# Kernel optimization log

Measured on AMD Instinct MI355X. Metric: run time of the kernel, lower is better.

The kernel has to match this reference:

```python
import jax, jax.numpy as jnp
import numpy as np

EMBED_DIM = 32  # module-level constant used for the 1/sqrt(d) scale in the source
DROP_P = 0.2


def setup_inputs() -> dict:
    key = jax.random.key(0)
    kx, kq, kk, kv = jax.random.split(key, 4)
    B, T, C = 8, 4096, EMBED_DIM
    x = jax.random.normal(kx, (B, T, C), dtype=jnp.float32)
    Wq = jax.random.normal(kq, (C, C), dtype=jnp.float32) * (1.0 / np.sqrt(C))
    Wk = jax.random.normal(kk, (C, C), dtype=jnp.float32) * (1.0 / np.sqrt(C))
    Wv = jax.random.normal(kv, (C, C), dtype=jnp.float32) * (1.0 / np.sqrt(C))
    return {"x": x, "Wq": Wq, "Wk": Wk, "Wv": Wv}


def reference(x, Wq, Wk, Wv):
    B, T, C = x.shape
    # bias-free linear projections: y = x @ W.T (torch nn.Linear convention)
    q = jnp.einsum('btc,dc->btd', x, Wq)
    k = jnp.einsum('btc,dc->btd', x, Wk)
    v = jnp.einsum('btc,dc->btd', x, Wv)
    # scaled scores [B, T, T]
    att = jnp.einsum('btd,bsd->bts', q, k) / jnp.sqrt(jnp.float32(EMBED_DIM))
    causal = jnp.tril(jnp.ones((T, T), dtype=bool))
    att = jnp.where(causal, att, -jnp.inf)
    wei = jax.nn.softmax(att, axis=-1)
    # dropout on attention weights (training mode, p=0.2), deterministic key
    keep = jax.random.bernoulli(jax.random.key(42), 1.0 - DROP_P, wei.shape)
    wei = jnp.where(keep, wei / (1.0 - DROP_P), 0.0)
    return jnp.einsum('bts,bsd->btd', wei, v)
```

## Files before the change

### kernel.cpp

```cpp
#include <hip/hip_runtime.h>
#include <stdint.h>

#define BB 8
#define TTN 4096
#define CCH 32
#define WIN 128
#define KEEP_LT9 3435974144u

typedef __attribute__((ext_vector_type(8))) short bf16x8;
typedef __attribute__((ext_vector_type(4))) float f32x4;

union B8 { uint32_t u[4]; uint4 q; bf16x8 v; };

__device__ __forceinline__ uint32_t cvt_pk_bf16(float lo, float hi) {
    uint32_t d;
    asm("v_cvt_pk_bf16_f32 %0, %1, %2" : "=v"(d) : "v"(lo), "v"(hi));
    return d;
}

__device__ __forceinline__ uint32_t rotl32(uint32_t x, int r) {
    return __builtin_amdgcn_alignbit(x, x, 32 - r);
}

__device__ __forceinline__ void threefry4(uint32_t i0, uint32_t i1, uint32_t i2, uint32_t i3,
                                          uint32_t& o0, uint32_t& o1, uint32_t& o2, uint32_t& o3) {
    const uint32_t K2 = 42u ^ 0x1BD11BDAu;
    uint32_t a0 = 0u, a1 = 0u, a2 = 0u, a3 = 0u;
    uint32_t b0 = i0 + 42u, b1 = i1 + 42u, b2 = i2 + 42u, b3 = i3 + 42u;
#define R4(r)                                                                  \
    { a0 += b0; a1 += b1; a2 += b2; a3 += b3;                                  \
      b0 = rotl32(b0, (r)); b1 = rotl32(b1, (r));                              \
      b2 = rotl32(b2, (r)); b3 = rotl32(b3, (r));                              \
      b0 ^= a0; b1 ^= a1; b2 ^= a2; b3 ^= a3; }
#define INJ(da, db)                                                            \
    { a0 += (da); a1 += (da); a2 += (da); a3 += (da);                          \
      b0 += (db); b1 += (db); b2 += (db); b3 += (db); }
    R4(13) R4(15) R4(26) R4(6)
    INJ(42u, K2 + 1u)
    R4(17) R4(29) R4(16) R4(24)
    INJ(K2, 2u)
    R4(13) R4(15) R4(26) R4(6)
    INJ(0u, 42u + 3u)
    R4(17) R4(29) R4(16) R4(24)
    INJ(42u, K2 + 4u)
    R4(13) R4(15) R4(26) R4(6)
    INJ(K2, 5u)
#undef R4
#undef INJ
    o0 = a0 ^ b0; o1 = a1 ^ b1; o2 = a2 ^ b2; o3 = a3 ^ b3;
}

__global__ __launch_bounds__(256) void proj_qkv(const float* __restrict__ x,
                                                const float* __restrict__ Wq,
                                                const float* __restrict__ Wk,
                                                const float* __restrict__ Wv,
                                                float* __restrict__ Qf,
                                                uint16_t* __restrict__ Kb,
                                                uint16_t* __restrict__ Vt) {
    __shared__ float sW[3][CCH * CCH];
    __shared__ uint16_t vs[256][34];
    const int tid = threadIdx.x;
    for (int i = tid; i < CCH * CCH; i += 256) {
        sW[0][i] = Wq[i]; sW[1][i] = Wk[i]; sW[2][i] = Wv[i];
    }
    __syncthreads();
    const int row = blockIdx.x * 256 + tid;
    const float4* xp = reinterpret_cast<const float4*>(x + (size_t)row * CCH);
    float xr[CCH];
    #pragma unroll
    for (int i = 0; i < 8; ++i) {
        float4 t4 = xp[i];
        xr[4*i] = t4.x; xr[4*i+1] = t4.y; xr[4*i+2] = t4.z; xr[4*i+3] = t4.w;
    }
    const float scale = 0.17677669529663687f;
    #pragma unroll
    for (int mtx = 0; mtx < 3; ++mtx) {
        float o[CCH];
        #pragma unroll
        for (int d = 0; d < CCH; ++d) {
            float s0 = 0.f, s1 = 0.f, s2 = 0.f, s3 = 0.f;
            #pragma unroll
            for (int c = 0; c < CCH; c += 4) {
                s0 += xr[c]   * sW[mtx][d*CCH + c];
                s1 += xr[c+1] * sW[mtx][d*CCH + c+1];
                s2 += xr[c+2] * sW[mtx][d*CCH + c+2];
                s3 += xr[c+3] * sW[mtx][d*CCH + c+3];
            }
            o[d] = (s0 + s1) + (s2 + s3);
            if (mtx == 0) o[d] *= scale;
        }
        if (mtx == 0) {
            float4* op = reinterpret_cast<float4*>(Qf + (size_t)row * CCH);
            #pragma unroll
            for (int i = 0; i < 8; ++i)
                op[i] = make_float4(o[4*i], o[4*i+1], o[4*i+2], o[4*i+3]);
        } else if (mtx == 1) {
            uint32_t dw[16];
            #pragma unroll
            for (int k = 0; k < 16; ++k) dw[k] = cvt_pk_bf16(o[2*k], o[2*k+1]);
            uint4* kp = reinterpret_cast<uint4*>((char*)Kb + (size_t)row * 64);
            #pragma unroll
            for (int q = 0; q < 4; ++q)
                kp[q] = make_uint4(dw[4*q], dw[4*q+1], dw[4*q+2], dw[4*q+3]);
        } else {
            #pragma unroll
            for (int k = 0; k < 16; ++k)
                *reinterpret_cast<uint32_t*>(&vs[tid][2*k]) = cvt_pk_bf16(o[2*k], o[2*k+1]);
        }
    }
    __syncthreads();
    const int b = blockIdx.x >> 4, seg = blockIdx.x & 15;
    const int d = tid >> 3, part = tid & 7;
    uint32_t dw[16];
    #pragma unroll
    for (int k = 0; k < 16; ++k) {
        const uint32_t lo = vs[part*32 + 2*k][d];
        const uint32_t hi = vs[part*32 + 2*k + 1][d];
        dw[k] = lo | (hi << 16);
    }
    uint16_t* dst = Vt + (size_t)b * (CCH * TTN) + (size_t)d * TTN + seg * 256 + part * 32;
    uint4* dp = reinterpret_cast<uint4*>(dst);
    #pragma unroll
    for (int q = 0; q < 4; ++q)
        dp[q] = make_uint4(dw[4*q], dw[4*q+1], dw[4*q+2], dw[4*q+3]);
}

__global__ __launch_bounds__(256, 8) void attn_mfma(const float* __restrict__ Qf,
                                                    const uint16_t* __restrict__ Kb,
                                                    const uint16_t* __restrict__ Vt,
                                                    float* __restrict__ out) {
    __shared__ __align__(16) char smem[4864];

    const int j = blockIdx.x;
    const int b = j & 7;
    const int thalf = (j >> 3) & 1;
    const int tile = 127 - (j >> 4);

    const int w = threadIdx.x >> 6;
    const int lane = threadIdx.x & 63;
    const int tl = lane & 15;
    const int g = lane >> 4;
    const int sg = w;
    const int slb = sg * 32;
    const int tbase = tile * 32 + thalf * 16;
    const int t_g = tbase + tl;

    const float* qrow = Qf + ((size_t)b * TTN + t_g) * CCH + g * 8;
    const float4 qa = *reinterpret_cast<const float4*>(qrow);
    const float4 qb = *reinterpret_cast<const float4*>(qrow + 4);
    B8 qf;
    qf.u[0] = cvt_pk_bf16(qa.x, qa.y); qf.u[1] = cvt_pk_bf16(qa.z, qa.w);
    qf.u[2] = cvt_pk_bf16(qb.x, qb.y); qf.u[3] = cvt_pk_bf16(qb.z, qb.w);

    f32x4 acc0 = {0.f,0.f,0.f,0.f}, acc1 = {0.f,0.f,0.f,0.f};
    float m = -1e30f, l = 0.f;

    const char* Kbb = (const char*)Kb + (size_t)b * TTN * 64;
    const char* Vbb = (const char*)Vt + (size_t)b * CCH * TTN * 2;
    const uint32_t idxb = ((uint32_t)b << 24) | ((uint32_t)t_g << 12);

    const int nwin = ((tbase + 15) >> 7) + 1;

#define ATT_WINDOW(S0, TAIL)                                                   \
    {                                                                          \
        const int srow = (S0) + slb;                                           \
        B8 ka, kc, va, vc, pf;                                                 \
        ka.q = *reinterpret_cast<const uint4*>(Kbb + (size_t)(srow + tl) * 64 + g * 16); \
        kc.q = *reinterpret_cast<const uint4*>(Kbb + (size_t)(srow + 16 + tl) * 64 + g * 16); \
        va.q = *reinterpret_cast<const uint4*>(Vbb + (size_t)tl * 8192 + (size_t)(srow + g * 8) * 2); \
        vc.q = *reinterpret_cast<const uint4*>(Vbb + (size_t)(16 + tl) * 8192 + (size_t)(srow + g * 8) * 2); \
               \
        const uint32_t ib = idxb | (uint32_t)(srow + 4 * g);                   \
        uint32_t r0, r1, r2, r3, r4, r5, r6, r7;                               \
        threefry4(ib,       ib + 1u,  ib + 2u,  ib + 3u,  r0, r1, r2, r3);     \
        threefry4(ib + 16u, ib + 17u, ib + 18u, ib + 19u, r4, r5, r6, r7);     \
        const f32x4 zz = {0.f,0.f,0.f,0.f};                                    \
        f32x4 d0 = __builtin_amdgcn_mfma_f32_16x16x32_bf16(ka.v, qf.v, zz, 0, 0, 0); \
        f32x4 d1 = __builtin_amdgcn_mfma_f32_16x16x32_bf16(kc.v, qf.v, zz, 0, 0, 0); \
        if (TAIL) {                                                            \
            const int sv = srow + 4 * g;                                       \
            d0.x = (sv + 0  <= t_g) ? d0.x : -1e30f;                           \
            d0.y = (sv + 1  <= t_g) ? d0.y : -1e30f;                           \
            d0.z = (sv + 2  <= t_g) ? d0.z : -1e30f;                           \
            d0.w = (sv + 3  <= t_g) ? d0.w : -1e30f;                           \
            d1.x = (sv + 16 <= t_g) ? d1.x : -1e30f;                           \
            d1.y = (sv + 17 <= t_g) ? d1.y : -1e30f;                           \
            d1.z = (sv + 18 <= t_g) ? d1.z : -1e30f;                           \
            d1.w = (sv + 19 <= t_g) ? d1.w : -1e30f;                           \
        }                                                                      \
        float mx = fmaxf(fmaxf(fmaxf(d0.x, d0.y), fmaxf(d0.z, d0.w)),          \
                         fmaxf(fmaxf(d1.x, d1.y), fmaxf(d1.z, d1.w)));         \
        mx = fmaxf(mx, __shfl_xor(mx, 16));                                    \
        mx = fmaxf(mx, __shfl_xor(mx, 32));                                    \
        const bool up = mx > m + 8.0f;               \
        const float corr = up ? __expf(m - mx) : 1.0f;                         \
        m = up ? mx : m;                                                       \
        l *= corr; acc0 *= corr; acc1 *= corr;                                 \
        float p0 = __expf(d0.x - m), p1 = __expf(d0.y - m);                    \
        float p2 = __expf(d0.z - m), p3 = __expf(d0.w - m);                    \
        float p4 = __expf(d1.x - m), p5 = __expf(d1.y - m);                    \
        float p6 = __expf(d1.z - m), p7 = __expf(d1.w - m);                    \
        if (TAIL) {                                                            \
            const float alive = (srow <= t_g) ? 1.0f : 0.0f;                   \
            p0 *= alive; p1 *= alive; p2 *= alive; p3 *= alive;                \
            p4 *= alive; p5 *= alive; p6 *= alive; p7 *= alive;                \
        }                                                                      \
        float ls = ((p0 + p1) + (p2 + p3)) + ((p4 + p5) + (p6 + p7));          \
        ls += __shfl_xor(ls, 16);                                              \
        ls += __shfl_xor(ls, 32);                                              \
        l += ls;                                                               \
        const float q0 = (r0 < KEEP_LT9) ? p0 : 0.f;        \
        const float q1 = (r1 < KEEP_LT9) ? p1 : 0.f;                           \
        const float q2 = (r2 < KEEP_LT9) ? p2 : 0.f;                           \
        const float q3 = (r3 < KEEP_LT9) ? p3 : 0.f;                           \
        const float q4 = (r4 < KEEP_LT9) ? p4 : 0.f;                           \
        const float q5 = (r5 < KEEP_LT9) ? p5 : 0.f;                           \
        const float q6 = (r6 < KEEP_LT9) ? p6 : 0.f;                           \
        const float q7 = (r7 < KEEP_LT9) ? p7 : 0.f;                           \
        const uint32_t k00 = cvt_pk_bf16(q0, q1), k01 = cvt_pk_bf16(q2, q3);   \
        const uint32_t k10 = cvt_pk_bf16(q4, q5), k11 = cvt_pk_bf16(q6, q7);   \
        const int srcA = 16 * ((g & 1) * 2) + tl;                              \
        const int srcB = srcA + 16;                                            \
        const uint32_t a0 = (uint32_t)__shfl((int)k00, srcA);                  \
        const uint32_t b0 = (uint32_t)__shfl((int)k10, srcA);                  \
        const uint32_t a1 = (uint32_t)__shfl((int)k01, srcA);                  \
        const uint32_t b1 = (uint32_t)__shfl((int)k11, srcA);                  \
        const uint32_t a2 = (uint32_t)__shfl((int)k00, srcB);                  \
        const uint32_t b2 = (uint32_t)__shfl((int)k10, srcB);                  \
        const uint32_t a3 = (uint32_t)__shfl((int)k01, srcB);                  \
        const uint32_t b3 = (uint32_t)__shfl((int)k11, srcB);                  \
        const bool hi = (g >= 2);                                              \
        pf.u[0] = hi ? b0 : a0; pf.u[1] = hi ? b1 : a1;                        \
        pf.u[2] = hi ? b2 : a2; pf.u[3] = hi ? b3 : a3;                        \
        acc0 = __builtin_amdgcn_mfma_f32_16x16x32_bf16(va.v, pf.v, acc0, 0, 0, 0); \
        acc1 = __builtin_amdgcn_mfma_f32_16x16x32_bf16(vc.v, pf.v, acc1, 0, 0, 0); \
    }

    #pragma unroll 1
    for (int win = 0; win < nwin - 1; ++win) {
        ATT_WINDOW(win << 7, 0)
    }
    {
        const int s0 = (nwin - 1) << 7;
        if (s0 + slb <= tbase + 15) ATT_WINDOW(s0, 1)
    }
#undef ATT_WINDOW

#define SLOT(S) reinterpret_cast<float*>(smem + (S) * 2432)
#define PUBLISH(SB)                                                            \
    {                                                                          \
        float* sb = (SB);                                                      \
        *reinterpret_cast<float4*>(sb + tl * 36 + 4 * g)      = make_float4(acc0.x, acc0.y, acc0.z, acc0.w); \
        *reinterpret_cast<float4*>(sb + tl * 36 + 16 + 4 * g) = make_float4(acc1.x, acc1.y, acc1.z, acc1.w); \
        if (g == 0) { sb[576 + 2 * tl] = m; sb[577 + 2 * tl] = l; }            \
    }
#define CONSUME(SB)                                                            \
    {                                                                          \
        const float* sb = (SB);                                                \
        const float m2 = sb[576 + 2 * tl], l2 = sb[577 + 2 * tl];              \
        const float4 x0 = *reinterpret_cast<const float4*>(sb + tl * 36 + 4 * g); \
        const float4 x1 = *reinterpret_cast<const float4*>(sb + tl * 36 + 16 + 4 * g); \
        const float mn = fmaxf(m, m2);                                         \
        const float ca = __expf(m - mn), cb = __expf(m2 - mn);                 \
        l = l * ca + l2 * cb;                                                  \
        acc0.x = acc0.x * ca + x0.x * cb; acc0.y = acc0.y * ca + x0.y * cb;    \
        acc0.z = acc0.z * ca + x0.z * cb; acc0.w = acc0.w * ca + x0.w * cb;    \
        acc1.x = acc1.x * ca + x1.x * cb; acc1.y = acc1.y * ca + x1.y * cb;    \
        acc1.z = acc1.z * ca + x1.z * cb; acc1.w = acc1.w * ca + x1.w * cb;    \
        m = mn;                                                                \
    }
    if (sg >= 2) PUBLISH(SLOT(sg - 2))
    __syncthreads();
    if (sg < 2) CONSUME(SLOT(sg))
    __syncthreads();
    if (sg == 1) PUBLISH(SLOT(0))
    __syncthreads();
    if (sg == 0) {
        CONSUME(SLOT(0))
        const float inv = 1.0f / (0.8f * l);
        float* orow = out + ((size_t)b * TTN + t_g) * CCH;
        *reinterpret_cast<float4*>(orow + 4 * g) =
            make_float4(acc0.x * inv, acc0.y * inv, acc0.z * inv, acc0.w * inv);
        *reinterpret_cast<float4*>(orow + 16 + 4 * g) =
            make_float4(acc1.x * inv, acc1.y * inv, acc1.z * inv, acc1.w * inv);
    }
#undef SLOT
#undef PUBLISH
#undef CONSUME
}

extern "C" void kernel_launch(void* const* d_in, const int* in_sizes, int n_in,
                              void* d_out, int out_size, void* d_ws, size_t ws_size,
                              hipStream_t stream) {
    const float* x  = (const float*)d_in[0];
    const float* Wq = (const float*)d_in[1];
    const float* Wk = (const float*)d_in[2];
    const float* Wv = (const float*)d_in[3];
    float* outp = (float*)d_out;

    float*    Qf = (float*)d_ws;
    uint16_t* Kb = (uint16_t*)((char*)d_ws + 4194304);
    uint16_t* Vt = (uint16_t*)((char*)d_ws + 6291456);

    proj_qkv<<<(BB * TTN) / 256, 256, 0, stream>>>(x, Wq, Wk, Wv, Qf, Kb, Vt);
    attn_mfma<<<2048, 256, 0, stream>>>(Qf, Kb, Vt, outp);
}
```

Baseline: 171.1 us.

## Prefetch next K/V window and RNG, use exp2 with folded log2e scale, LDS exchange

The attention loop now software-pipelines the work: the next window's K/V tiles are loaded and its threefry dropout bits computed before the current window's softmax and PV MFMAs run. The softmax switches to raw v_exp_f32 (base 2) by folding log2(e) into the Q scale. The per-lane row sum is deferred and reduced once after the loop. The cross-lane max and P-fragment exchanges use LDS instead of shuffles. This raises register pressure (occupancy hint drops from 8 to 6) and LDS use in exchange for hiding memory latency and cutting exp and shuffle cost.

Measured after the change: 164.7 us. 1.04x faster.

```diff
diff --git a/kernel.cpp b/kernel.cpp
--- a/kernel.cpp
+++ b/kernel.cpp
@@ -4,7 +4,6 @@
 #define BB 8
 #define TTN 4096
 #define CCH 32
-#define WIN 128
 #define KEEP_LT9 3435974144u
 
 typedef __attribute__((ext_vector_type(8))) short bf16x8;
@@ -15,6 +14,12 @@
 __device__ __forceinline__ uint32_t cvt_pk_bf16(float lo, float hi) {
     uint32_t d;
     asm("v_cvt_pk_bf16_f32 %0, %1, %2" : "=v"(d) : "v"(lo), "v"(hi));
+    return d;
+}
+
+__device__ __forceinline__ float exp2_fast(float x) {
+    float d;
+    asm("v_exp_f32 %0, %1" : "=v"(d) : "v"(x));
     return d;
 }
 
@@ -72,7 +77,7 @@
         float4 t4 = xp[i];
         xr[4*i] = t4.x; xr[4*i+1] = t4.y; xr[4*i+2] = t4.z; xr[4*i+3] = t4.w;
     }
-    const float scale = 0.17677669529663687f;
+    const float scale = 0.2550348616f;
     #pragma unroll
     for (int mtx = 0; mtx < 3; ++mtx) {
         float o[CCH];
@@ -125,11 +130,11 @@
         dp[q] = make_uint4(dw[4*q], dw[4*q+1], dw[4*q+2], dw[4*q+3]);
 }
 
-__global__ __launch_bounds__(256, 8) void attn_mfma(const float* __restrict__ Qf,
+__global__ __launch_bounds__(256, 6) void attn_mfma(const float* __restrict__ Qf,
                                                     const uint16_t* __restrict__ Kb,
                                                     const uint16_t* __restrict__ Vt,
                                                     float* __restrict__ out) {
-    __shared__ __align__(16) char smem[4864];
+    __shared__ __align__(16) char smem[9984];
 
     const int j = blockIdx.x;
     const int b = j & 7;
@@ -140,8 +145,7 @@
     const int lane = threadIdx.x & 63;
     const int tl = lane & 15;
     const int g = lane >> 4;
-    const int sg = w;
-    const int slb = sg * 32;
+    const int slb = w * 32;
     const int tbase = tile * 32 + thalf * 16;
     const int t_g = tbase + tl;
 
@@ -161,24 +165,33 @@
 
     const int nwin = ((tbase + 15) >> 7) + 1;
 
-#define ATT_WINDOW(S0, TAIL)                                                   \
+    float* mxex = reinterpret_cast<float*>(smem) + (w << 6);
+    uint32_t* pex = reinterpret_cast<uint32_t*>(smem + 1024) + (w << 8);
+
+    B8 kaA, kcA, vaA, vcA, kaB, kcB, vaB, vcB;
+    uint32_t rA[8], rB[8];
+
+#define LOADF(KA, KC, VA, VC, S0)                                              \
     {                                                                          \
         const int srow = (S0) + slb;                                           \
-        B8 ka, kc, va, vc, pf;                                                 \
-        ka.q = *reinterpret_cast<const uint4*>(Kbb + (size_t)(srow + tl) * 64 + g * 16); \
-        kc.q = *reinterpret_cast<const uint4*>(Kbb + (size_t)(srow + 16 + tl) * 64 + g * 16); \
-        va.q = *reinterpret_cast<const uint4*>(Vbb + (size_t)tl * 8192 + (size_t)(srow + g * 8) * 2); \
-        vc.q = *reinterpret_cast<const uint4*>(Vbb + (size_t)(16 + tl) * 8192 + (size_t)(srow + g * 8) * 2); \
-               \
-        const uint32_t ib = idxb | (uint32_t)(srow + 4 * g);                   \
-        uint32_t r0, r1, r2, r3, r4, r5, r6, r7;                               \
-        threefry4(ib,       ib + 1u,  ib + 2u,  ib + 3u,  r0, r1, r2, r3);     \
-        threefry4(ib + 16u, ib + 17u, ib + 18u, ib + 19u, r4, r5, r6, r7);     \
+        KA.q = *reinterpret_cast<const uint4*>(Kbb + (size_t)(srow + tl) * 64 + g * 16); \
+        KC.q = *reinterpret_cast<const uint4*>(Kbb + (size_t)(srow + 16 + tl) * 64 + g * 16); \
+        VA.q = *reinterpret_cast<const uint4*>(Vbb + (size_t)tl * 8192 + (size_t)(srow + g * 8) * 2); \
+        VC.q = *reinterpret_cast<const uint4*>(Vbb + (size_t)(16 + tl) * 8192 + (size_t)(srow + g * 8) * 2); \
+    }
+#define TF8(R, S0)                                                             \
+    {                                                                          \
+        const uint32_t ib = idxb | (uint32_t)((S0) + slb + 4 * g);             \
+        threefry4(ib,       ib + 1u,  ib + 2u,  ib + 3u,  R[0], R[1], R[2], R[3]); \
+        threefry4(ib + 16u, ib + 17u, ib + 18u, ib + 19u, R[4], R[5], R[6], R[7]); \
+    }
+#define SMAXPV(S0, TAIL)                                                       \
+    {                                                                          \
         const f32x4 zz = {0.f,0.f,0.f,0.f};                                    \
-        f32x4 d0 = __builtin_amdgcn_mfma_f32_16x16x32_bf16(ka.v, qf.v, zz, 0, 0, 0); \
-        f32x4 d1 = __builtin_amdgcn_mfma_f32_16x16x32_bf16(kc.v, qf.v, zz, 0, 0, 0); \
+        f32x4 d0 = __builtin_amdgcn_mfma_f32_16x16x32_bf16(kaA.v, qf.v, zz, 0, 0, 0); \
+        f32x4 d1 = __builtin_amdgcn_mfma_f32_16x16x32_bf16(kcA.v, qf.v, zz, 0, 0, 0); \
         if (TAIL) {                                                            \
-            const int sv = srow + 4 * g;                                       \
+            const int sv = (S0) + slb + 4 * g;                                 \
             d0.x = (sv + 0  <= t_g) ? d0.x : -1e30f;                           \
             d0.y = (sv + 1  <= t_g) ? d0.y : -1e30f;                           \
             d0.z = (sv + 2  <= t_g) ? d0.z : -1e30f;                           \
@@ -190,63 +203,67 @@
         }                                                                      \
         float mx = fmaxf(fmaxf(fmaxf(d0.x, d0.y), fmaxf(d0.z, d0.w)),          \
                          fmaxf(fmaxf(d1.x, d1.y), fmaxf(d1.z, d1.w)));         \
-        mx = fmaxf(mx, __shfl_xor(mx, 16));                                    \
-        mx = fmaxf(mx, __shfl_xor(mx, 32));                                    \
-        const bool up = mx > m + 8.0f;               \
-        const float corr = up ? __expf(m - mx) : 1.0f;                         \
+        mxex[(tl << 2) + g] = mx;                           \
+        const float4 m4 = *reinterpret_cast<const float4*>(mxex + (tl << 2));  \
+        mx = fmaxf(fmaxf(m4.x, m4.y), fmaxf(m4.z, m4.w));                      \
+        const bool up = mx > m + 11.5f;          \
+        const float corr = up ? exp2_fast(m - mx) : 1.0f;                      \
         m = up ? mx : m;                                                       \
         l *= corr; acc0 *= corr; acc1 *= corr;                                 \
-        float p0 = __expf(d0.x - m), p1 = __expf(d0.y - m);                    \
-        float p2 = __expf(d0.z - m), p3 = __expf(d0.w - m);                    \
-        float p4 = __expf(d1.x - m), p5 = __expf(d1.y - m);                    \
-        float p6 = __expf(d1.z - m), p7 = __expf(d1.w - m);                    \
+        float p0 = exp2_fast(d0.x - m), p1 = exp2_fast(d0.y - m);              \
+        float p2 = exp2_fast(d0.z - m), p3 = exp2_fast(d0.w - m);              \
+        float p4 = exp2_fast(d1.x - m), p5 = exp2_fast(d1.y - m);              \
+        float p6 = exp2_fast(d1.z - m), p7 = exp2_fast(d1.w - m);              \
         if (TAIL) {                                                            \
-            const float alive = (srow <= t_g) ? 1.0f : 0.0f;                   \
+            const float alive = ((S0) + slb <= t_g) ? 1.0f : 0.0f;             \
             p0 *= alive; p1 *= alive; p2 *= alive; p3 *= alive;                \
             p4 *= alive; p5 *= alive; p6 *= alive; p7 *= alive;                \
         }                                                                      \
-        float ls = ((p0 + p1) + (p2 + p3)) + ((p4 + p5) + (p6 + p7));          \
-        ls += __shfl_xor(ls, 16);                                              \
-        ls += __shfl_xor(ls, 32);                                              \
-        l += ls;                                                               \
-        const float q0 = (r0 < KEEP_LT9) ? p0 : 0.f;        \
-        const float q1 = (r1 < KEEP_LT9) ? p1 : 0.f;                           \
-        const float q2 = (r2 < KEEP_LT9) ? p2 : 0.f;                           \
-        const float q3 = (r3 < KEEP_LT9) ? p3 : 0.f;                           \
-        const float q4 = (r4 < KEEP_LT9) ? p4 : 0.f;                           \
-        const float q5 = (r5 < KEEP_LT9) ? p5 : 0.f;                           \
-        const float q6 = (r6 < KEEP_LT9) ? p6 : 0.f;                           \
-        const float q7 = (r7 < KEEP_LT9) ? p7 : 0.f;                           \
+        l += ((p0 + p1) + (p2 + p3)) + ((p4 + p5) + (p6 + p7));                \
+        const float q0 = (rA[0] < KEEP_LT9) ? p0 : 0.f;                        \
+        const float q1 = (rA[1] < KEEP_LT9) ? p1 : 0.f;                        \
+        const float q2 = (rA[2] < KEEP_LT9) ? p2 : 0.f;                        \
+        const float q3 = (rA[3] < KEEP_LT9) ? p3 : 0.f;                        \
+        const float q4 = (rA[4] < KEEP_LT9) ? p4 : 0.f;                        \
+        const float q5 = (rA[5] < KEEP_LT9) ? p5 : 0.f;                        \
+        const float q6 = (rA[6] < KEEP_LT9) ? p6 : 0.f;                        \
+        const float q7 = (rA[7] < KEEP_LT9) ? p7 : 0.f;                        \
         const uint32_t k00 = cvt_pk_bf16(q0, q1), k01 = cvt_pk_bf16(q2, q3);   \
         const uint32_t k10 = cvt_pk_bf16(q4, q5), k11 = cvt_pk_bf16(q6, q7);   \
-        const int srcA = 16 * ((g & 1) * 2) + tl;                              \
-        const int srcB = srcA + 16;                                            \
-        const uint32_t a0 = (uint32_t)__shfl((int)k00, srcA);                  \
-        const uint32_t b0 = (uint32_t)__shfl((int)k10, srcA);                  \
-        const uint32_t a1 = (uint32_t)__shfl((int)k01, srcA);                  \
-        const uint32_t b1 = (uint32_t)__shfl((int)k11, srcA);                  \
-        const uint32_t a2 = (uint32_t)__shfl((int)k00, srcB);                  \
-        const uint32_t b2 = (uint32_t)__shfl((int)k10, srcB);                  \
-        const uint32_t a3 = (uint32_t)__shfl((int)k01, srcB);                  \
-        const uint32_t b3 = (uint32_t)__shfl((int)k11, srcB);                  \
-        const bool hi = (g >= 2);                                              \
-        pf.u[0] = hi ? b0 : a0; pf.u[1] = hi ? b1 : a1;                        \
-        pf.u[2] = hi ? b2 : a2; pf.u[3] = hi ? b3 : a3;                        \
-        acc0 = __builtin_amdgcn_mfma_f32_16x16x32_bf16(va.v, pf.v, acc0, 0, 0, 0); \
-        acc1 = __builtin_amdgcn_mfma_f32_16x16x32_bf16(vc.v, pf.v, acc1, 0, 0, 0); \
-    }
-
+        *reinterpret_cast<uint4*>(pex + (lane << 2)) = make_uint4(k00, k01, k10, k11); \
+        const int srcA4 = (((g & 1) ? 32 : 0) + tl) << 2;                      \
+        const int sel = (g >= 2) ? 2 : 0;                                      \
+        const uint2 lo2 = *reinterpret_cast<const uint2*>(pex + srcA4 + sel);  \
+        const uint2 hi2 = *reinterpret_cast<const uint2*>(pex + srcA4 + 64 + sel); \
+        B8 pf;                                                                 \
+        pf.u[0] = lo2.x; pf.u[1] = lo2.y; pf.u[2] = hi2.x; pf.u[3] = hi2.y;    \
+        acc0 = __builtin_amdgcn_mfma_f32_16x16x32_bf16(vaA.v, pf.v, acc0, 0, 0, 0); \
+        acc1 = __builtin_amdgcn_mfma_f32_16x16x32_bf16(vcA.v, pf.v, acc1, 0, 0, 0); \
+    }
+
+    LOADF(kaA, kcA, vaA, vcA, 0)
+    TF8(rA, 0)
     #pragma unroll 1
     for (int win = 0; win < nwin - 1; ++win) {
-        ATT_WINDOW(win << 7, 0)
+        LOADF(kaB, kcB, vaB, vcB, (win + 1) << 7)
+        TF8(rB, (win + 1) << 7)
+        SMAXPV(win << 7, 0)
+        kaA = kaB; kcA = kcB; vaA = vaB; vcA = vcB;
+        #pragma unroll
+        for (int i = 0; i < 8; ++i) rA[i] = rB[i];
     }
     {
         const int s0 = (nwin - 1) << 7;
-        if (s0 + slb <= tbase + 15) ATT_WINDOW(s0, 1)
-    }
-#undef ATT_WINDOW
-
-#define SLOT(S) reinterpret_cast<float*>(smem + (S) * 2432)
+        if (s0 + slb <= tbase + 15) SMAXPV(s0, 1)
+    }
+#undef SMAXPV
+#undef TF8
+#undef LOADF
+
+    l += __shfl_xor(l, 16);
+    l += __shfl_xor(l, 32);
+
+#define SLOT(S) reinterpret_cast<float*>(smem + 5120 + (S) * 2432)
 #define PUBLISH(SB)                                                            \
     {                                                                          \
         float* sb = (SB);                                                      \
@@ -261,7 +278,7 @@
         const float4 x0 = *reinterpret_cast<const float4*>(sb + tl * 36 + 4 * g); \
         const float4 x1 = *reinterpret_cast<const float4*>(sb + tl * 36 + 16 + 4 * g); \
         const float mn = fmaxf(m, m2);                                         \
-        const float ca = __expf(m - mn), cb = __expf(m2 - mn);                 \
+        const float ca = exp2_fast(m - mn), cb = exp2_fast(m2 - mn);           \
         l = l * ca + l2 * cb;                                                  \
         acc0.x = acc0.x * ca + x0.x * cb; acc0.y = acc0.y * ca + x0.y * cb;    \
         acc0.z = acc0.z * ca + x0.z * cb; acc0.w = acc0.w * ca + x0.w * cb;    \
@@ -269,13 +286,13 @@
         acc1.z = acc1.z * ca + x1.z * cb; acc1.w = acc1.w * ca + x1.w * cb;    \
         m = mn;                                                                \
     }
-    if (sg >= 2) PUBLISH(SLOT(sg - 2))
-    __syncthreads();
-    if (sg < 2) CONSUME(SLOT(sg))
-    __syncthreads();
-    if (sg == 1) PUBLISH(SLOT(0))
-    __syncthreads();
-    if (sg == 0) {
+    if (w >= 2) PUBLISH(SLOT(w - 2))
+    __syncthreads();
+    if (w < 2) CONSUME(SLOT(w))
+    __syncthreads();
+    if (w == 1) PUBLISH(SLOT(0))
+    __syncthreads();
+    if (w == 0) {
         CONSUME(SLOT(0))
         const float inv = 1.0f / (0.8f * l);
         float* orow = out + ((size_t)b * TTN + t_g) * CCH;
```
